# Kernel optimization log

Measured on AMD Instinct MI355X. Metric: run time of the kernel, lower is better.

Reference implementation:

```python
import jax, jax.numpy as jnp
import numpy as np
import math

B, T, D = 2, 512, 1024
H, HD = 16, 64
F = 4096
L = 2
R = 32
LOOP_DIM = 64
TEMB = 256
MAXIT = 8
TOPK = 0.55
EPS = 1e-6


def _ste(x, q):
    # straight-through estimator: forward = q, backward = identity
    return x + jax.lax.stop_gradient(q - x)


def bitlinear(x, w, topk_ratio=None):
    # BitNet b1.58 fake-quant: ternary weights (per-tensor absmean scale),
    # int8 per-token absmax activations; optional topk activation sparsity.
    s = jnp.mean(jnp.abs(w)) + 1e-8
    wq = _ste(w, jnp.clip(jnp.round(w / s), -1.0, 1.0) * s)
    if topk_ratio is not None:
        k = max(1, int(math.ceil(topk_ratio * x.shape[-1])))
        ax = jnp.abs(x)
        thr = jax.lax.top_k(ax, k)[0][..., -1:]
        x = jnp.where(ax >= thr, x, 0.0)
    a = jnp.maximum(jnp.max(jnp.abs(x), axis=-1, keepdims=True), 1e-8)
    xq = _ste(x, jnp.clip(jnp.round(x * (127.0 / a)), -128.0, 127.0) * (a / 127.0))
    return xq @ wq.T


def rmsnorm(x, w):
    return x * jax.lax.rsqrt(jnp.mean(x * x, axis=-1, keepdims=True) + EPS) * w


def _rope(x):
    # x: (B,H,T,HD)
    half = HD // 2
    inv = 1.0 / (10000.0 ** (jnp.arange(half, dtype=jnp.float32) / half))
    ang = jnp.arange(x.shape[2], dtype=jnp.float32)[:, None] * inv[None, :]
    cos, sin = jnp.cos(ang), jnp.sin(ang)
    x1, x2 = x[..., :half], x[..., half:]
    return jnp.concatenate([x1 * cos - x2 * sin, x1 * sin + x2 * cos], axis=-1)


def bitblock(h, n1, wq, wk, wv, wo, n2, wg, wu, wd):
    # pre-norm attention + SwiGLU FFN, all projections BitLinear
    b, t, _ = h.shape
    a_in = rmsnorm(h, n1)
    heads = lambda p: p.reshape(b, t, H, HD).transpose(0, 2, 1, 3)
    q = _rope(heads(bitlinear(a_in, wq)))
    k = _rope(heads(bitlinear(a_in, wk)))
    v = heads(bitlinear(a_in, wv))
    scores = jnp.einsum('bhqd,bhkd->bhqk', q, k) / math.sqrt(HD)
    mask = jnp.tril(jnp.ones((t, t), dtype=bool))
    attn = jax.nn.softmax(jnp.where(mask, scores, -1e9), axis=-1)
    o = jnp.einsum('bhqk,bhkd->bhqd', attn, v).transpose(0, 2, 1, 3).reshape(b, t, D)
    h = h + bitlinear(o, wo)
    f_in = rmsnorm(h, n2)
    h = h + bitlinear(jax.nn.silu(bitlinear(f_in, wg)) * bitlinear(f_in, wu), wd)
    return h


def loop_delta(i, t_emb, lp_w, lp2_w, lp2_b):
    # loop_index_inject: sinusoidal loop signal gated by t_emb, padded to D
    half = LOOP_DIM // 2
    frac = i / max(MAXIT - 1, 1)
    freqs = jnp.exp(-math.log(10000.0) * jnp.arange(half, dtype=jnp.float32) / half)
    ang = frac * freqs
    sig = jnp.concatenate([jnp.sin(ang), jnp.cos(ang)])  # (LOOP_DIM,)
    comb = sig[None, :] * (t_emb @ lp_w.T) + (t_emb @ lp2_w.T + lp2_b)  # (B,LOOP_DIM)
    return jnp.pad(comb, ((0, 0), (0, D - LOOP_DIM)))[:, None, :]  # (B,1,D)


def setup_inputs() -> dict:
    key = jax.random.key(0)
    ks = jax.random.split(key, 24)
    g = lambda k, shape, sc=0.02: sc * jax.random.normal(k, shape, dtype=jnp.float32)
    return {
        'x': jax.random.normal(ks[0], (B, T, D), dtype=jnp.float32),
        'e': jax.random.normal(ks[1], (B, T, D), dtype=jnp.float32),
        't_emb': jax.random.normal(ks[2], (B, TEMB), dtype=jnp.float32),
        'blk_norm1': jnp.ones((L, D), jnp.float32),
        'blk_wq': g(ks[3], (L, D, D)),
        'blk_wk': g(ks[4], (L, D, D)),
        'blk_wv': g(ks[5], (L, D, D)),
        'blk_wo': g(ks[6], (L, D, D)),
        'blk_norm2': jnp.ones((L, D), jnp.float32),
        'blk_wg': g(ks[7], (L, F, D)),
        'blk_wu': g(ks[8], (L, F, D)),
        'blk_wd': g(ks[9], (L, D, F)),
        'A_raw': 0.1 * jax.random.normal(ks[10], (D,), dtype=jnp.float32),
        'B_w': g(ks[11], (D, D)),
        'lora_down': g(ks[12], (R, D)),
        'lora_up': g(ks[13], (D, R)),
        'iter_gate': jnp.full((MAXIT,), 0.1, jnp.float32),
        'act_w': g(ks[14], (1, D)),
        'alpha': jnp.full((MAXIT,), 1.0 / L, jnp.float32),
        'loop_proj_w': g(ks[15], (LOOP_DIM, TEMB)),
        'loop_proj2_w': g(ks[16], (LOOP_DIM, TEMB)),
        'loop_proj2_b': jnp.zeros((LOOP_DIM,), jnp.float32),
        'loop_norm_w': jnp.ones((D,), jnp.float32),
        'n_loops': 8,
    }


def reference(x, e, t_emb, blk_norm1, blk_wq, blk_wk, blk_wv, blk_wo,
              blk_norm2, blk_wg, blk_wu, blk_wd, A_raw, B_w,
              lora_down, lora_up, iter_gate, act_w, alpha,
              loop_proj_w, loop_proj2_w, loop_proj2_b, loop_norm_w, n_loops):
    A_eff = 0.99 * jnp.tanh(A_raw)          # diagonal LTI, |A|<0.99
    Be = bitlinear(e, B_w)                  # loop-invariant anchor B(e)
    h = x
    h_out = x
    ws = []
    for i in range(int(n_loops)):
        h_in = rmsnorm(h + loop_delta(i, t_emb, loop_proj_w, loop_proj2_w, loop_proj2_b), loop_norm_w)
        bo = h_in
        for l in range(L):
            bo = bitblock(bo, blk_norm1[l], blk_wq[l], blk_wk[l], blk_wv[l], blk_wo[l],
                          blk_norm2[l], blk_wg[l], blk_wu[l], blk_wd[l])
        bo = alpha[i] * bo
        h = A_eff * h + Be + bo             # LTI injection
        h = h + iter_gate[i] * bitlinear(bitlinear(h, lora_down), lora_up, topk_ratio=TOPK)
        w = jax.nn.sigmoid(bitlinear(h, act_w))  # (B,T,1) soft ACT weight
        h_out = h_out + w * (h - h_out)     # incremental residual blend
        ws.append(w)
    ponder = jnp.mean(jnp.stack(ws))
    return h_out, ponder
```

## Files before the change

### kernel.cpp

```cpp
#include <hip/hip_runtime.h>
#include <stdint.h>

#define DEV static __device__ __forceinline__

typedef float f32x4 __attribute__((ext_vector_type(4)));
typedef int   i32x4 __attribute__((ext_vector_type(4)));
typedef unsigned short u16x8 __attribute__((ext_vector_type(8)));

DEV float bf2f(unsigned short u){ return __uint_as_float(((unsigned int)u)<<16); }
DEV unsigned short f2bfr(float f){
  unsigned int u = __float_as_uint(f);
  return (unsigned short)((u + 0x7FFF + ((u>>16)&1)) >> 16);
}
DEV signed char f2i8(float f){ return (signed char)(int)f; }

DEV float wredsum(float v){
#pragma unroll
  for (int o=32;o;o>>=1) v += __shfl_xor(v,o);
  return v;
}
DEV float wredmax(float v){
#pragma unroll
  for (int o=32;o;o>>=1) v = fmaxf(v,__shfl_xor(v,o));
  return v;
}
DEV float bredsum(float v, float* red){
  v = wredsum(v);
  if ((threadIdx.x&63)==0) red[threadIdx.x>>6] = v;
  __syncthreads();
  float r = red[0]+red[1]+red[2]+red[3];
  __syncthreads();
  return r;
}
DEV float bredmax(float v, float* red){
  v = wredmax(v);
  if ((threadIdx.x&63)==0) red[threadIdx.x>>6] = v;
  __syncthreads();
  float r = fmaxf(fmaxf(red[0],red[1]),fmaxf(red[2],red[3]));
  __syncthreads();
  return r;
}

__global__ void fill_k(float* p, int n, float v){
  int i = blockIdx.x*256 + threadIdx.x;
  if (i < n) p[i] = v;
}

__global__ __launch_bounds__(256) void setup_misc_k(const float* __restrict__ x,
                                                    float* __restrict__ h, float* __restrict__ ho,
                                                    const float* __restrict__ temb,
                                                    const float* __restrict__ lpw,
                                                    const float* __restrict__ lp2w,
                                                    const float* __restrict__ lp2b,
                                                    float* __restrict__ delta,
                                                    float* __restrict__ tab){
  __shared__ float red[4];
  int bid = blockIdx.x, t = threadIdx.x;
  if (bid < 1024){
    int i = bid*256 + t;
    float4 v = *(const float4*)(x + (size_t)i*4);
    *(float4*)(h  + (size_t)i*4) = v;
    *(float4*)(ho + (size_t)i*4) = v;
    if (i==0) ho[1048576] = 0.f;
  } else if (bid < 1152){
    int blk = bid - 1024;
    int b = blk >> 6, j = blk & 63;
    float te = temb[b*256 + t];
    float p1 = bredsum(te * lpw[j*256 + t], red);
    float p2 = bredsum(te * lp2w[j*256 + t], red);
    if (t < 8){
      int i = t;
      float frac = (float)i / 7.f;
      int jj = j & 31;
      float fr = expf(-logf(10000.f) * (float)jj * (1.f/32.f));
      float ang = frac * fr;
      float sig = (j < 32) ? sinf(ang) : cosf(ang);
      delta[i*128 + b*64 + j] = sig*p1 + p2 + lp2b[j];
    }
  } else {
    int i = (bid-1152)*256 + t;
    int tpos = i >> 5, d = i & 31;
    float inv = powf(10000.f, -(float)d * (1.f/32.f));
    float sv, cv; sincosf((float)tpos * inv, &sv, &cv);
    tab[i*2]   = cv;
    tab[i*2+1] = sv;
  }
}

struct WSetup {
  const float* src[18];
  signed char* dst[18];
  int mode[18];
};
DEV long n4of(int mat){ return mat<9 ? 262144 : (mat<15 ? 1048576 : (mat<17 ? 8192 : 256)); }

__global__ __launch_bounds__(256) void absmean_all_k(WSetup wsu, float* __restrict__ part){
  __shared__ float red[4];
  int bid = blockIdx.x, mat, seg;
  if (bid < 2304){ mat = bid >> 8; seg = bid & 255; }
  else if (bid < 8448){ mat = 9 + ((bid-2304) >> 10); seg = (bid-2304) & 1023; }
  else { mat = 15 + ((bid-8448) >> 8); seg = (bid-8448) & 255; }
  long n4 = n4of(mat);
  int segs = (mat >= 9 && mat < 15) ? 1024 : 256;
  long cnt = n4 / segs;
  const float4* p = (const float4*)wsu.src[mat] + (long)seg*cnt;
  float s0=0.f, s1=0.f, s2=0.f, s3=0.f;
  if (cnt >= 1024){
    long quar = cnt >> 2;
    const float4* p1 = p + quar;
    const float4* p2 = p + 2*quar;
    const float4* p3 = p + 3*quar;
    for (long j = threadIdx.x; j < quar; j += 256){
      float4 a = p[j], b = p1[j], c = p2[j], d = p3[j];
      s0 += fabsf(a.x)+fabsf(a.y)+fabsf(a.z)+fabsf(a.w);
      s1 += fabsf(b.x)+fabsf(b.y)+fabsf(b.z)+fabsf(b.w);
      s2 += fabsf(c.x)+fabsf(c.y)+fabsf(c.z)+fabsf(c.w);
      s3 += fabsf(d.x)+fabsf(d.y)+fabsf(d.z)+fabsf(d.w);
    }
  } else {
    for (long j = threadIdx.x; j < cnt; j += 256){
      float4 a = p[j];
      s0 += fabsf(a.x)+fabsf(a.y)+fabsf(a.z)+fabsf(a.w);
    }
  }
  float s = bredsum(s0+s1+s2+s3, red);
  if (threadIdx.x==0) part[(long)mat*1024 + seg] = s;
}

__global__ __launch_bounds__(256) void finalize_scales_k(const float* __restrict__ part,
                                                         float* __restrict__ scales){
  __shared__ float red[4];
  const long numel[18] = {1048576, 1048576,1048576, 1048576,1048576, 1048576,1048576,
                          1048576,1048576, 4194304,4194304, 4194304,4194304, 4194304,4194304,
                          32768, 32768, 1024};
  int t = threadIdx.x;
  for (int m=0;m<18;m++){
    int segs = (m >= 9 && m < 15) ? 1024 : 256;
    float v = 0.f;
    for (int j=t; j<segs; j+=256) v += part[(long)m*1024 + j];
    v = bredsum(v, red);
    if (t==0) scales[m] = v/(float)numel[m] + 1e-8f;
  }
  if (t==0){
    for (int l=0;l<2;l++){
      scales[18+l*3+0] = scales[1+l];
      scales[18+l*3+1] = scales[3+l];
      scales[18+l*3+2] = scales[5+l];
      scales[24+l*2+0] = scales[9+l];
      scales[24+l*2+1] = scales[11+l];
    }
  }
}

__global__ __launch_bounds__(256) void quantw_all_k(WSetup wsu, const float* __restrict__ scales){
  int bid = blockIdx.x;
  int mat = 0, c = 0;
  for (;;){
    int nb = mat<9 ? 256 : (mat<15 ? 1024 : (mat<17 ? 8 : 1));
    if (bid < c + nb) break;
    c += nb; mat++;
  }
  long seg = bid - c;
  long n4 = n4of(mat);
  float s = scales[mat];
  int md = wsu.mode[mat];
  const float4* src = (const float4*)wsu.src[mat];
  char4* dst = (char4*)wsu.dst[mat];
  long base = seg*1024;
#pragma unroll
  for (int k=0;k<4;k++){
    long i = base + k*256 + threadIdx.x;
    if (i < n4){
      float4 v = src[i];
      char4 q;
      q.x = f2i8(fminf(fmaxf(rintf(v.x/s), -1.f), 1.f));
      q.y = f2i8(fminf(fmaxf(rintf(v.y/s), -1.f), 1.f));
      q.z = f2i8(fminf(fmaxf(rintf(v.z/s), -1.f), 1.f));
      q.w = f2i8(fminf(fmaxf(rintf(v.w/s), -1.f), 1.f));
      if (md == 0) dst[i] = q;
      else {
        long r = i >> 8, cc = i & 255;
        dst[(((r<<1) | (md-1))<<8) | cc] = q;
      }
    }
  }
}

template<bool BF>
__global__ __launch_bounds__(256) void rowquant1k_k(const void* __restrict__ xin,
                                                    signed char* __restrict__ xq,
                                                    float* __restrict__ rs){
  __shared__ float red[4];
  int m = blockIdx.x, t = threadIdx.x;
  float v[4];
  if (BF){
    ushort4 u = *(const ushort4*)((const unsigned short*)xin + (size_t)m*1024 + t*4);
    v[0]=bf2f(u.x); v[1]=bf2f(u.y); v[2]=bf2f(u.z); v[3]=bf2f(u.w);
  } else {
    float4 f = *(const float4*)((const float*)xin + (size_t)m*1024 + t*4);
    v[0]=f.x; v[1]=f.y; v[2]=f.z; v[3]=f.w;
  }
  float am = fmaxf(fmaxf(fabsf(v[0]),fabsf(v[1])),fmaxf(fabsf(v[2]),fabsf(v[3])));
  am = bredmax(am, red);
  float a = fmaxf(am, 1e-8f), inv = 127.f/a;
  char4 q;
  q.x = f2i8(fminf(fmaxf(rintf(v[0]*inv),-128.f),127.f));
  q.y = f2i8(fminf(fmaxf(rintf(v[1]*inv),-128.f),127.f));
  q.z = f2i8(fminf(fmaxf(rintf(v[2]*inv),-128.f),127.f));
  q.w = f2i8(fminf(fmaxf(rintf(v[3]*inv),-128.f),127.f));
  *(char4*)(xq + (size_t)m*1024 + t*4) = q;
  if (t==0) rs[m] = a/127.f;
}

__global__ __launch_bounds__(256) void rowquant4k_k(const unsigned short* __restrict__ x,
                                                    signed char* __restrict__ xq,
                                                    float* __restrict__ rs){
  __shared__ float red[4];
  int m = blockIdx.x, t = threadIdx.x;
  const unsigned short* p = x + (size_t)m*4096 + t*16;
  u16x8 u0 = *(const u16x8*)p;
  u16x8 u1 = *(const u16x8*)(p + 8);
  float v[16];
#pragma unroll
  for (int j=0;j<8;j++){ v[j] = bf2f(u0[j]); v[j+8] = bf2f(u1[j]); }
  float am = 0.f;
#pragma unroll
  for (int j=0;j<16;j++) am = fmaxf(am, fabsf(v[j]));
  am = bredmax(am, red);
  float a = fmaxf(am, 1e-8f), inv = 127.f/a;
#pragma unroll
  for (int j=0;j<16;j+=4){
    char4 q;
    q.x = f2i8(fminf(fmaxf(rintf(v[j+0]*inv),-128.f),127.f));
    q.y = f2i8(fminf(fmaxf(rintf(v[j+1]*inv),-128.f),127.f));
    q.z = f2i8(fminf(fmaxf(rintf(v[j+2]*inv),-128.f),127.f));
    q.w = f2i8(fminf(fmaxf(rintf(v[j+3]*inv),-128.f),127.f));
    *(char4*)(xq + (size_t)m*4096 + t*16 + j) = q;
  }
  if (t==0) rs[m] = a/127.f;
}

__global__ __launch_bounds__(256) void loopnorm_quant_k(const float* __restrict__ h,
                                                        const float* __restrict__ delta,
                                                        const float* __restrict__ lnw,
                                                        const float* __restrict__ n1,
                                                        float* __restrict__ hin,
                                                        signed char* __restrict__ xq,
                                                        float* __restrict__ rs){
  __shared__ float red[4];
  int m = blockIdx.x, t = threadIdx.x;
  int b = m >> 9;
  float v[4];
  float4 f = *(const float4*)(h + (size_t)m*1024 + t*4);
  v[0]=f.x; v[1]=f.y; v[2]=f.z; v[3]=f.w;
  if (t < 16){
#pragma unroll
    for (int j=0;j<4;j++) v[j] += delta[b*64 + t*4 + j];
  }
  float ss = v[0]*v[0]+v[1]*v[1]+v[2]*v[2]+v[3]*v[3];
  ss = bredsum(ss, red);
  float r1 = rsqrtf(ss*(1.f/1024.f) + 1e-6f);
  float w4[4];
#pragma unroll
  for (int j=0;j<4;j++) w4[j] = v[j]*r1*lnw[t*4+j];
  float4 of; of.x=w4[0]; of.y=w4[1]; of.z=w4[2]; of.w=w4[3];
  *(float4*)(hin + (size_t)m*1024 + t*4) = of;
  float s2 = w4[0]*w4[0]+w4[1]*w4[1]+w4[2]*w4[2]+w4[3]*w4[3];
  s2 = bredsum(s2, red);
  float r2 = rsqrtf(s2*(1.f/1024.f) + 1e-6f);
  float y[4];
#pragma unroll
  for (int j=0;j<4;j++) y[j] = w4[j]*r2*n1[t*4+j];
  float am = fmaxf(fmaxf(fabsf(y[0]),fabsf(y[1])),fmaxf(fabsf(y[2]),fabsf(y[3])));
  am = bredmax(am, red);
  float a = fmaxf(am, 1e-8f), inv = 127.f/a;
  char4 q;
  q.x = f2i8(fminf(fmaxf(rintf(y[0]*inv),-128.f),127.f));
  q.y = f2i8(fminf(fmaxf(rintf(y[1]*inv),-128.f),127.f));
  q.z = f2i8(fminf(fmaxf(rintf(y[2]*inv),-128.f),127.f));
  q.w = f2i8(fminf(fmaxf(rintf(y[3]*inv),-128.f),127.f));
  *(char4*)(xq + (size_t)m*1024 + t*4) = q;
  if (t==0) rs[m] = a/127.f;
}

DEV f32x4 accfence(f32x4 c){ asm volatile("s_nop 7\n\ts_nop 7" : "+v"(c)); return c; }
DEV i32x4 accfencei(i32x4 c){ asm volatile("s_nop 7\n\ts_nop 7" : "+v"(c)); return c; }

template<bool SPLITK, bool GUSILU>
__global__ __launch_bounds__(256)
void gemm_i8(const signed char* __restrict__ A, const signed char* __restrict__ W,
             const float* __restrict__ rowsc, const float* __restrict__ wscv,
             const float* __restrict__ res, float* __restrict__ C, int N, int Kf, int Kc)
{
  __shared__ __align__(16) signed char As[3][8192];
  __shared__ __align__(16) signed char Bs[3][8192];
  const int tid = threadIdx.x;
  const int lane = tid & 63, wvid = tid >> 6;
  const int wr = wvid >> 1, wc = wvid & 1;
  const int bm = blockIdx.y, bn = blockIdx.x;

  const int r0 = (wvid<<4) + (lane>>2);
  const int sw = (((lane&3) ^ ((r0>>1)&3)) << 4);
  const long kstart = SPLITK ? (long)blockIdx.z * Kc : 0;
  const signed char* gA = A + (size_t)(bm*128 + r0)*Kf + kstart + sw;
  const signed char* gB = W + (size_t)(bn*128 + r0)*Kf + kstart + sw;
  const size_t row64 = (size_t)64*Kf;

#define STAGE(buf, koff) do { \
    __builtin_amdgcn_global_load_lds(gA + (koff),         &As[buf][(wvid<<10)],      16, 0, 0); \
    __builtin_amdgcn_global_load_lds(gA + (koff) + row64, &As[buf][(wvid<<10)+4096], 16, 0, 0); \
    __builtin_amdgcn_global_load_lds(gB + (koff),         &Bs[buf][(wvid<<10)],      16, 0, 0); \
    __builtin_amdgcn_global_load_lds(gB + (koff) + row64, &Bs[buf][(wvid<<10)+4096], 16, 0, 0); \
  } while(0)

  i32x4 acc[4][4] = {};
  const int rA = (wr<<6) + (lane&15);
  const int rB = (wc<<6) + (lane&15);
  const int psA = (((lane>>4) ^ (((lane&15)>>1)&3)) << 4);

  const int NT = Kc >> 6;
  STAGE(0, 0);
  STAGE(1, 64);
  int cur = 0, nxt = 1, nx2 = 2;
  for (int kt = 0; kt < NT; ++kt){
    const int k2 = kt + 2;
    const int kn = (k2 < NT) ? (k2<<6) : 0;
    STAGE(nx2, kn);
    asm volatile("s_waitcnt vmcnt(8)" ::: "memory");
    __builtin_amdgcn_s_barrier();
    asm volatile("" ::: "memory");
    i32x4 a[4], b[4];
    const signed char* Ab = As[cur];
    const signed char* Bb = Bs[cur];
#pragma unroll
    for (int mi=0;mi<4;mi++) a[mi] = *(const i32x4*)(Ab + (rA + mi*16)*64 + psA);
#pragma unroll
    for (int ni=0;ni<4;ni++) b[ni] = *(const i32x4*)(Bb + (rB + ni*16)*64 + psA);
#pragma unroll
    for (int mi=0;mi<4;mi++)
#pragma unroll
      for (int ni=0;ni<4;ni++)
        asm("v_mfma_i32_16x16x64_i8 %0, %1, %2, %0" : "+v"(acc[mi][ni]) : "v"(a[mi]), "v"(b[ni]));
    asm volatile("s_waitcnt lgkmcnt(0)" ::: "memory");
    __builtin_amdgcn_s_barrier();
    int tmp = cur; cur = nxt; nxt = nx2; nx2 = tmp;
  }
#undef STAGE

#pragma unroll
  for (int mi=0;mi<4;mi++)
#pragma unroll
    for (int ni=0;ni<4;ni++)
      acc[mi][ni] = accfencei(acc[mi][ni]);

  const int rif = (lane>>4)<<2;
  const int cif = lane&15;
  const int gcol0 = bn*128 + (wc<<6);

  if constexpr (SPLITK){
    float* P = C + (size_t)blockIdx.z * ((size_t)N << 10);
#pragma unroll
    for (int mi=0;mi<4;mi++)
#pragma unroll
      for (int r=0;r<4;r++){
        const int grow = bm*128 + (wr<<6) + mi*16 + rif + r;
#pragma unroll
        for (int ni=0;ni<4;ni++)
          P[(size_t)grow*N + gcol0 + ni*16 + cif] = (float)acc[mi][ni][r];
      }
    return;
  }

  if constexpr (GUSILU){
    const float sg = wscv[0], su = wscv[1];
    unsigned short* Cb = (unsigned short*)C;
#pragma unroll
    for (int mi=0;mi<4;mi++){
#pragma unroll
      for (int r=0;r<4;r++){
        const int grow = bm*128 + (wr<<6) + mi*16 + rif + r;
        const float rsc = rowsc[grow];
#pragma unroll
        for (int ni=0;ni<4;ni++){
          const int gcol = gcol0 + ni*16 + cif;
          float val = (float)acc[mi][ni][r] * rsc * ((gcol & 1) ? su : sg);
          float other = __shfl_xor(val, 1);
          if (!(lane & 1)){
            float g = val, u = other;
            float outv = g/(1.f+expf(-g))*u;
            Cb[(size_t)grow*4096 + (gcol>>1)] = f2bfr(outv);
          }
        }
      }
    }
    return;
  }

#pragma unroll
  for (int mi=0;mi<4;mi++){
#pragma unroll
    for (int r=0;r<4;r++){
      const int grow = bm*128 + (wr<<6) + mi*16 + rif + r;
      const float rsc = rowsc[grow];
#pragma unroll
      for (int ni=0;ni<4;ni++){
        const int gcol = gcol0 + ni*16 + cif;
        float vvv = (float)acc[mi][ni][r] * rsc * wscv[0];
        const size_t off = (size_t)grow*N + gcol;
        if (res) vvv += res[off];
        C[off] = vvv;
      }
    }
  }
}

__global__ __launch_bounds__(256)
void gemm_qkv128(const signed char* __restrict__ A, const signed char* __restrict__ W,
                 const float* __restrict__ rowsc, const float* __restrict__ wscv,
                 const float* __restrict__ tab, unsigned short* __restrict__ C)
{
  __shared__ __align__(16) signed char As[3][8192];
  __shared__ __align__(16) signed char Bs[3][8192];
  const int tid = threadIdx.x;
  const int lane = tid & 63, wvid = tid >> 6;
  const int wr = wvid >> 1, wc = wvid & 1;
  const int bm = blockIdx.y, bn = blockIdx.x;
  const int Kf = 1024;

  const int r0 = (wvid<<4) + (lane>>2);
  const int sw = (((lane&3) ^ ((r0>>1)&3)) << 4);
  const signed char* gA = A + (size_t)(bm*128 + r0)*Kf + sw;
  const signed char* gB = W + (size_t)(bn*128 + r0)*Kf + sw;
  const size_t row64 = (size_t)64*Kf;

#define STAGE(buf, koff) do { \
    __builtin_amdgcn_global_load_lds(gA + (koff),         &As[buf][(wvid<<10)],      16, 0, 0); \
    __builtin_amdgcn_global_load_lds(gA + (koff) + row64, &As[buf][(wvid<<10)+4096], 16, 0, 0); \
    __builtin_amdgcn_global_load_lds(gB + (koff),         &Bs[buf][(wvid<<10)],      16, 0, 0); \
    __builtin_amdgcn_global_load_lds(gB + (koff) + row64, &Bs[buf][(wvid<<10)+4096], 16, 0, 0); \
  } while(0)

  i32x4 acc[4][4] = {};
  const int rA = (wr<<6) + (lane&15);
  const int rB = (wc<<6) + (lane&15);
  const int psA = (((lane>>4) ^ (((lane&15)>>1)&3)) << 4);

  const int NT = 16;
  STAGE(0, 0);
  STAGE(1, 64);
  int cur = 0, nxt = 1, nx2 = 2;
  for (int kt = 0; kt < NT; ++kt){
    const int k2 = kt + 2;
    const int kn = (k2 < NT) ? (k2<<6) : 0;
    STAGE(nx2, kn);
    asm volatile("s_waitcnt vmcnt(8)" ::: "memory");
    __builtin_amdgcn_s_barrier();
    asm volatile("" ::: "memory");
    i32x4 a[4], b[4];
    const signed char* Ab = As[cur];
    const signed char* Bb = Bs[cur];
#pragma unroll
    for (int mi=0;mi<4;mi++) a[mi] = *(const i32x4*)(Ab + (rA + mi*16)*64 + psA);
#pragma unroll
    for (int ni=0;ni<4;ni++) b[ni] = *(const i32x4*)(Bb + (rB + ni*16)*64 + psA);
#pragma unroll
    for (int mi=0;mi<4;mi++)
#pragma unroll
      for (int ni=0;ni<4;ni++)
        asm("v_mfma_i32_16x16x64_i8 %0, %1, %2, %0" : "+v"(acc[mi][ni]) : "v"(a[mi]), "v"(b[ni]));
    asm volatile("s_waitcnt lgkmcnt(0)" ::: "memory");
    __builtin_amdgcn_s_barrier();
    int tmp = cur; cur = nxt; nxt = nx2; nx2 = tmp;
  }
#undef STAGE

#pragma unroll
  for (int mi=0;mi<4;mi++)
#pragma unroll
    for (int ni=0;ni<4;ni++)
      acc[mi][ni] = accfencei(acc[mi][ni]);

  const int rif = (lane>>4)<<2;
  const int cif = lane&15;
  const int gcol0 = bn*128 + (wc<<6);
  const int sec = gcol0 >> 10;
  const float wsc = wscv[sec] * ((sec==0) ? 0.125f : 1.f);

  if (sec < 2){
#pragma unroll
    for (int mi=0;mi<4;mi++){
#pragma unroll
      for (int r=0;r<4;r++){
        const int grow = bm*128 + (wr<<6) + mi*16 + rif + r;
        const float s = rowsc[grow] * wsc;
        const int tpos = grow & 511;
#pragma unroll
        for (int np=0;np<2;np++){
          const int d = np*16 + cif;
          float2 cs = *(const float2*)(tab + (size_t)((tpos<<5) + d)*2);
          float x1 = (float)acc[mi][np][r]   * s;
          float x2 = (float)acc[mi][np+2][r] * s;
          C[(size_t)grow*3072 + gcol0 + d]      = f2bfr(x1*cs.x - x2*cs.y);
          C[(size_t)grow*3072 + gcol0 + 32 + d] = f2bfr(x1*cs.y + x2*cs.x);
        }
      }
    }
  } else {
#pragma unroll
    for (int mi=0;mi<4;mi++){
#pragma unroll
      for (int r=0;r<4;r++){
        const int grow = bm*128 + (wr<<6) + mi*16 + rif + r;
        const float s = rowsc[grow] * wsc;
#pragma unroll
        for (int ni=0;ni<4;ni++)
          C[(size_t)grow*3072 + gcol0 + ni*16 + cif] = f2bfr((float)acc[mi][ni][r] * s);
      }
    }
  }
}

__global__ __launch_bounds__(256) void reduce4_k(const float* __restrict__ P,
                                                 const float* __restrict__ rowsc,
                                                 const float* __restrict__ wsc,
                                                 const float* __restrict__ res,
                                                 float* __restrict__ C){
  int m = blockIdx.x, t = threadIdx.x;
  float s0 = rowsc[m] * wsc[0];
  size_t off = (size_t)m*1024 + t*4;
  float4 a = *(const float4*)(P + off);
  float4 b = *(const float4*)(P + 1048576 + off);
  float4 c = *(const float4*)(P + 2097152 + off);
  float4 d = *(const float4*)(P + 3145728 + off);
  float4 o;
  o.x = (a.x+b.x+c.x+d.x)*s0;
  o.y = (a.y+b.y+c.y+d.y)*s0;
  o.z = (a.z+b.z+c.z+d.z)*s0;
  o.w = (a.w+b.w+c.w+d.w)*s0;
  if (res){
    float4 r = *(const float4*)(res + off);
    o.x += r.x; o.y += r.y; o.z += r.z; o.w += r.w;
  }
  *(float4*)(C + off) = o;
}

__global__ __launch_bounds__(256) void redq_norm_k(const float* __restrict__ P,
                                                   const float* rowsc,
                                                   const float* __restrict__ wsc,
                                                   const float* __restrict__ res,
                                                   const float* __restrict__ gamma,
                                                   float* __restrict__ Cout,
                                                   signed char* __restrict__ xq,
                                                   float* rs){
  __shared__ float red[4];
  int m = blockIdx.x, t = threadIdx.x;
  float s0 = rowsc[m] * wsc[0];
  size_t off = (size_t)m*1024 + t*4;
  float4 a = *(const float4*)(P + off);
  float4 b = *(const float4*)(P + 1048576 + off);
  float4 c = *(const float4*)(P + 2097152 + off);
  float4 d = *(const float4*)(P + 3145728 + off);
  float4 r4 = *(const float4*)(res + off);
  float v[4];
  v[0] = r4.x + (a.x+b.x+c.x+d.x)*s0;
  v[1] = r4.y + (a.y+b.y+c.y+d.y)*s0;
  v[2] = r4.z + (a.z+b.z+c.z+d.z)*s0;
  v[3] = r4.w + (a.w+b.w+c.w+d.w)*s0;
  float4 of; of.x=v[0]; of.y=v[1]; of.z=v[2]; of.w=v[3];
  *(float4*)(Cout + off) = of;
  float ss = v[0]*v[0]+v[1]*v[1]+v[2]*v[2]+v[3]*v[3];
  ss = bredsum(ss, red);
  float r1 = rsqrtf(ss*(1.f/1024.f) + 1e-6f);
  float y[4];
#pragma unroll
  for (int j=0;j<4;j++) y[j] = v[j]*r1*gamma[t*4+j];
  float am = fmaxf(fmaxf(fabsf(y[0]),fabsf(y[1])),fmaxf(fabsf(y[2]),fabsf(y[3])));
  am = bredmax(am, red);
  float aq = fmaxf(am, 1e-8f), inv = 127.f/aq;
  char4 q;
  q.x = f2i8(fminf(fmaxf(rintf(y[0]*inv),-128.f),127.f));
  q.y = f2i8(fminf(fmaxf(rintf(y[1]*inv),-128.f),127.f));
  q.z = f2i8(fminf(fmaxf(rintf(y[2]*inv),-128.f),127.f));
  q.w = f2i8(fminf(fmaxf(rintf(y[3]*inv),-128.f),127.f));
  *(char4*)(xq + (size_t)m*1024 + t*4) = q;
  if (t==0) rs[m] = aq/127.f;
}

__global__ __launch_bounds__(256) void redfin_k(const float* __restrict__ P,
                                                const float* __restrict__ rowsc,
                                                const float* __restrict__ wsc,
                                                const float* __restrict__ res,
                                                float* __restrict__ h,
                                                const float* __restrict__ Be,
                                                const float* __restrict__ Araw,
                                                const float* __restrict__ alpha, int it,
                                                const signed char* __restrict__ ldq,
                                                const float* __restrict__ sld,
                                                const signed char* __restrict__ luq,
                                                const float* __restrict__ slu,
                                                const signed char* __restrict__ actq,
                                                const float* __restrict__ sact,
                                                const float* __restrict__ ig,
                                                float* __restrict__ hout,
                                                float* __restrict__ ponder,
                                                const float* __restrict__ dnext,
                                                const float* __restrict__ lnw,
                                                const float* __restrict__ n1,
                                                float* __restrict__ hin,
                                                signed char* __restrict__ xqn,
                                                float* __restrict__ rsn,
                                                int doNext){
  __shared__ float red[4];
  __shared__ float xrow[1024];
  __shared__ float part[256];
  __shared__ float xs[32];
  __shared__ float sh_thr, sh_gs;
  int m = blockIdx.x, t = threadIdx.x;
  float al = alpha[it];
  float s0 = rowsc[m] * wsc[0];
  size_t off = (size_t)m*1024 + t*4;
  float4 a = *(const float4*)(P + off);
  float4 b = *(const float4*)(P + 1048576 + off);
  float4 c = *(const float4*)(P + 2097152 + off);
  float4 d = *(const float4*)(P + 3145728 + off);
  float4 r4 = *(const float4*)(res + off);
  float4 hh = *(const float4*)(h + off);
  float4 be = *(const float4*)(Be + off);
  float4 ar = *(const float4*)(Araw + t*4);
  float v[4];
  v[0] = 0.99f*tanhf(ar.x)*hh.x + be.x + al*(r4.x + (a.x+b.x+c.x+d.x)*s0);
  v[1] = 0.99f*tanhf(ar.y)*hh.y + be.y + al*(r4.y + (a.y+b.y+c.y+d.y)*s0);
  v[2] = 0.99f*tanhf(ar.z)*hh.z + be.z + al*(r4.z + (a.z+b.z+c.z+d.z)*s0);
  v[3] = 0.99f*tanhf(ar.w)*hh.w + be.w + al*(r4.w + (a.w+b.w+c.w+d.w)*s0);
  float am = fmaxf(fmaxf(fabsf(v[0]),fabsf(v[1])),fmaxf(fabsf(v[2]),fabsf(v[3])));
  am = bredmax(am, red);
  float aq = fmaxf(am, 1e-8f), inv = 127.f/aq;
#pragma unroll
  for (int j=0;j<4;j++) xrow[t*4+j] = fminf(fmaxf(rintf(v[j]*inv),-128.f),127.f);
  float rsv = aq/127.f;
  __syncthreads();
  {
    int r = t & 31, seg = t >> 5;
    const signed char* wrow = ldq + (size_t)r*1024 + seg*128;
    const float* xr = xrow + seg*128;
    float acc = 0.f;
    for (int k=0;k<128;k+=4){
      char4 w4 = *(const char4*)(wrow + k);
      acc += xr[k]*(float)w4.x + xr[k+1]*(float)w4.y + xr[k+2]*(float)w4.z + xr[k+3]*(float)w4.w;
    }
    part[t] = acc;
  }
  __syncthreads();
  if (t < 32){
    float s = 0.f;
    for (int sg=0; sg<8; sg++) s += part[sg*32 + t];
    xs[t] = s * rsv * (*sld);
  }
  __syncthreads();
  float val = 0.f, av = 0.f, amax = 0.f;
  if (t < 32){
    val = xs[t]; av = fabsf(val);
    int rank = 0;
    for (int j=0;j<32;j++){
      float aj = fabsf(xs[j]);
      amax = fmaxf(amax, aj);
      if (aj > av || (aj == av && j < t)) rank++;
    }
    if (rank == 17) sh_thr = av;
  }
  __syncthreads();
  if (t < 32){
    float a2 = fmaxf(amax, 1e-8f);
    float q = 0.f;
    if (av >= sh_thr) q = fminf(fmaxf(rintf(val*(127.f/a2)), -128.f), 127.f);
    xs[t] = q;
    if (t == 0) sh_gs = ig[it] * (*slu) * (a2/127.f);
  }
  __syncthreads();
  float gs = sh_gs;
  float hn[4];
  int n0 = t*4;
#pragma unroll
  for (int ni=0;ni<4;ni++){
    const signed char* lr = luq + (size_t)(n0+ni)*32;
    float dd = 0.f;
    for (int k=0;k<32;k+=4){
      char4 w4 = *(const char4*)(lr + k);
      dd += xs[k]*(float)w4.x + xs[k+1]*(float)w4.y + xs[k+2]*(float)w4.z + xs[k+3]*(float)w4.w;
    }
    hn[ni] = v[ni] + gs*dd;
  }
  float am2 = fmaxf(fmaxf(fabsf(hn[0]),fabsf(hn[1])),fmaxf(fabsf(hn[2]),fabsf(hn[3])));
  am2 = bredmax(am2, red);
  float a2 = fmaxf(am2, 1e-8f), inv2 = 127.f/a2;
  float zp = 0.f;
#pragma unroll
  for (int ni=0;ni<4;ni++){
    float q = fminf(fmaxf(rintf(hn[ni]*inv2),-128.f),127.f);
    zp += q * (float)actq[n0+ni];
  }
  zp = bredsum(zp, red);
  float z = zp * (a2/127.f) * (*sact);
  float wv = 1.f/(1.f+expf(-z));
#pragma unroll
  for (int ni=0;ni<4;ni++){
    size_t o2 = (size_t)m*1024 + n0+ni;
    float ho = hout[o2];
    hout[o2] = ho + wv*(hn[ni]-ho);
    h[o2] = hn[ni];
  }
  if (t==0) atomicAdd(ponder, wv * (1.f/8192.f));

  if (doNext){
    int b2 = m >> 9;
    float v2[4] = {hn[0], hn[1], hn[2], hn[3]};
    if (t < 16){
#pragma unroll
      for (int j=0;j<4;j++) v2[j] += dnext[b2*64 + t*4 + j];
    }
    float ss2 = v2[0]*v2[0]+v2[1]*v2[1]+v2[2]*v2[2]+v2[3]*v2[3];
    ss2 = bredsum(ss2, red);
    float r1 = rsqrtf(ss2*(1.f/1024.f) + 1e-6f);
    float w4[4];
#pragma unroll
    for (int j=0;j<4;j++) w4[j] = v2[j]*r1*lnw[t*4+j];
    float4 of; of.x=w4[0]; of.y=w4[1]; of.z=w4[2]; of.w=w4[3];
    *(float4*)(hin + off) = of;
    float s2 = w4[0]*w4[0]+w4[1]*w4[1]+w4[2]*w4[2]+w4[3]*w4[3];
    s2 = bredsum(s2, red);
    float r2 = rsqrtf(s2*(1.f/1024.f) + 1e-6f);
    float y[4];
#pragma unroll
    for (int j=0;j<4;j++) y[j] = w4[j]*r2*n1[t*4+j];
    float am3 = fmaxf(fmaxf(fabsf(y[0]),fabsf(y[1])),fmaxf(fabsf(y[2]),fabsf(y[3])));
    am3 = bredmax(am3, red);
    float aq3 = fmaxf(am3, 1e-8f), inv3 = 127.f/aq3;
    char4 q;
    q.x = f2i8(fminf(fmaxf(rintf(y[0]*inv3),-128.f),127.f));
    q.y = f2i8(fminf(fmaxf(rintf(y[1]*inv3),-128.f),127.f));
    q.z = f2i8(fminf(fmaxf(rintf(y[2]*inv3),-128.f),127.f));
    q.w = f2i8(fminf(fmaxf(rintf(y[3]*inv3),-128.f),127.f));
    *(char4*)(xqn + off) = q;
    if (t==0) rsn[m] = aq3/127.f;
  }
}

DEV int swz64(int r, int c){ return r*64 + (c ^ ((r&7)<<3)); }

__global__ __launch_bounds__(256) void attn_bf16_k(const unsigned short* __restrict__ qkv,
                                                   unsigned short* __restrict__ o){
  __shared__ __align__(16) unsigned short Qs[4096];
  __shared__ __align__(16) unsigned short Ks[4096];
  __shared__ __align__(16) unsigned short Vt[4096];
  __shared__ __align__(16) unsigned short Ps[4][1024];
  const int tid = threadIdx.x;
  const int lane = tid & 63, wv = tid >> 6;
  const int qt = blockIdx.x & 7, bh = blockIdx.x >> 3;
  const int b = bh >> 4, h = bh & 15;
  const int tokb = b*512;
  const int l15 = lane & 15, lh = lane >> 4;

  {
    int r = tid >> 2, c0 = (tid & 3) << 4;
    const unsigned short* s = qkv + (size_t)(tokb + qt*64 + r)*3072 + h*64 + c0;
    u16x8 f0 = *(const u16x8*)s, f1 = *(const u16x8*)(s+8);
    *(u16x8*)(Qs + swz64(r, c0))   = f0;
    *(u16x8*)(Qs + swz64(r, c0+8)) = f1;
  }

  float m_run[4] = {-1e30f,-1e30f,-1e30f,-1e30f};
  float l_run[4] = {0.f,0.f,0.f,0.f};
  f32x4 accO[4] = {};

  for (int kt = 0; kt <= qt; ++kt){
    __syncthreads();
    {
      int r = tid >> 2, c0 = (tid & 3) << 4;
      const unsigned short* s = qkv + (size_t)(tokb + kt*64 + r)*3072 + 1024 + h*64 + c0;
      u16x8 f0 = *(const u16x8*)s, f1 = *(const u16x8*)(s+8);
      *(u16x8*)(Ks + swz64(r, c0))   = f0;
      *(u16x8*)(Ks + swz64(r, c0+8)) = f1;
    }
    {
      int r0 = (tid >> 3) << 1, cv = (tid & 7) << 3;
      const unsigned short* s0 = qkv + (size_t)(tokb + kt*64 + r0)*3072 + 2048 + h*64 + cv;
      u16x8 a = *(const u16x8*)s0;
      u16x8 b2 = *(const u16x8*)(s0 + 3072);
#pragma unroll
      for (int j=0;j<8;j++){
        int d = cv + j;
        unsigned int pk = (unsigned int)a[j] | ((unsigned int)b2[j]<<16);
        *(unsigned int*)(Vt + swz64(d, r0)) = pk;
      }
    }
    __syncthreads();

    f32x4 s4[4] = {};
#pragma unroll
    for (int kc=0; kc<2; ++kc){
      i32x4 aq = *(const i32x4*)(Qs + swz64(wv*16 + l15, kc*32 + lh*8));
#pragma unroll
      for (int nt=0; nt<4; ++nt){
        i32x4 bk = *(const i32x4*)(Ks + swz64(nt*16 + l15, kc*32 + lh*8));
        asm("v_mfma_f32_16x16x32_bf16 %0, %1, %2, %0" : "+v"(s4[nt]) : "v"(aq), "v"(bk));
      }
    }
#pragma unroll
    for (int nt=0; nt<4; ++nt) s4[nt] = accfence(s4[nt]);

    const bool diag = (kt == qt);
    float sf[4];
#pragma unroll
    for (int r=0;r<4;r++){
      int rl = lh*4 + r;
      float mx = -1e30f;
#pragma unroll
      for (int nt=0; nt<4; ++nt){
        float v = s4[nt][r];
        if (diag && (nt*16 + l15) > (wv*16 + rl)) v = -1e30f;
        s4[nt][r] = v;
        mx = fmaxf(mx, v);
      }
      mx = fmaxf(mx, __shfl_xor(mx,1));
      mx = fmaxf(mx, __shfl_xor(mx,2));
      mx = fmaxf(mx, __shfl_xor(mx,4));
      mx = fmaxf(mx, __shfl_xor(mx,8));
      float mn = fmaxf(m_run[r], mx);
      sf[r] = __expf(m_run[r] - mn);
      m_run[r] = mn;
      float ps = 0.f;
#pragma unroll
      for (int nt=0; nt<4; ++nt){
        float p = __expf(s4[nt][r] - mn);
        ps += p;
        Ps[wv][swz64(rl, nt*16 + l15)] = f2bfr(p);
      }
      ps += __shfl_xor(ps,1); ps += __shfl_xor(ps,2);
      ps += __shfl_xor(ps,4); ps += __shfl_xor(ps,8);
      l_run[r] = l_run[r]*sf[r] + ps;
    }
#pragma unroll
    for (int dt=0; dt<4; ++dt){
#pragma unroll
      for (int r=0;r<4;r++) accO[dt][r] *= sf[r];
      accO[dt] = accfence(accO[dt]);
    }
#pragma unroll
    for (int kc=0; kc<2; ++kc){
      i32x4 pa = *(const i32x4*)(Ps[wv] + swz64(l15, kc*32 + lh*8));
#pragma unroll
      for (int dt=0; dt<4; ++dt){
        i32x4 vb3 = *(const i32x4*)(Vt + swz64(dt*16 + l15, kc*32 + lh*8));
        asm("v_mfma_f32_16x16x32_bf16 %0, %1, %2, %0" : "+v"(accO[dt]) : "v"(pa), "v"(vb3));
      }
    }
  }
#pragma unroll
  for (int dt=0; dt<4; ++dt) accO[dt] = accfence(accO[dt]);
#pragma unroll
  for (int r=0;r<4;r++){
    float invl = 1.f / l_run[r];
    int row = qt*64 + wv*16 + lh*4 + r;
    unsigned short* op = o + (size_t)(tokb + row)*1024 + h*64 + l15;
#pragma unroll
    for (int dt=0; dt<4; ++dt)
      op[dt*16] = f2bfr(accO[dt][r] * invl);
  }
}

extern "C" void kernel_launch(void* const* d_in, const int* in_sizes, int n_in,
                              void* d_out, int out_size, void* d_ws, size_t ws_size,
                              hipStream_t stream)
{
  (void)in_sizes; (void)n_in;
  const float* x     = (const float*)d_in[0];
  const float* e     = (const float*)d_in[1];
  const float* temb  = (const float*)d_in[2];
  const float* bn1   = (const float*)d_in[3];
  const float* bwq   = (const float*)d_in[4];
  const float* bwk   = (const float*)d_in[5];
  const float* bwv   = (const float*)d_in[6];
  const float* bwo   = (const float*)d_in[7];
  const float* bn2   = (const float*)d_in[8];
  const float* bwg   = (const float*)d_in[9];
  const float* bwu   = (const float*)d_in[10];
  const float* bwd   = (const float*)d_in[11];
  const float* Araw  = (const float*)d_in[12];
  const float* Bw    = (const float*)d_in[13];
  const float* ldw   = (const float*)d_in[14];
  const float* luw   = (const float*)d_in[15];
  const float* ig    = (const float*)d_in[16];
  const float* actw  = (const float*)d_in[17];
  const float* alph  = (const float*)d_in[18];
  const float* lpw   = (const float*)d_in[19];
  const float* lp2w  = (const float*)d_in[20];
  const float* lp2b  = (const float*)d_in[21];
  const float* lnw   = (const float*)d_in[22];

  char* ws = (char*)d_ws;
  float* out = (float*)d_out;
  const size_t WS_NEEDED = 94600704ull;
  if (ws_size < WS_NEEDED){
    fill_k<<<(out_size+255)/256,256,0,stream>>>(out, out_size, 1.0e9f);
    return;
  }

  signed char* qw_qkv = (signed char*)(ws + 0);
  signed char* qw_wo  = (signed char*)(ws + 6291456);
  signed char* qw_gu  = (signed char*)(ws + 8388608);
  signed char* qw_wd  = (signed char*)(ws + 25165824);
  signed char* qw_bw  = (signed char*)(ws + 33554432);
  signed char* qw_ld  = (signed char*)(ws + 34603008);
  signed char* qw_lu  = (signed char*)(ws + 34635776);
  signed char* qw_act = (signed char*)(ws + 34668544);
  float* scales = (float*)(ws + 34669568);
  float* delta  = (float*)(ws + 34688512);
  float* hbuf   = (float*)(ws + 34692608);
  float* Bebuf  = (float*)(ws + 38886912);
  float* bufX   = (float*)(ws + 43081216);
  float* bufY   = (float*)(ws + 47275520);
  float* gub    = (float*)(ws + 51469824);
  unsigned short* qkv_bf = (unsigned short*)(ws + 76635648);
  unsigned short* obuf = (unsigned short*)(ws + 85024256);
  signed char* xq1k = (signed char*)(ws + 89218560);
  float* rs1k   = (float*)(ws + 90267136);
  signed char* xqm  = (signed char*)(ws + 90271232);
  float* rsm    = (float*)(ws + 94465536);
  float* ropetab= (float*)(ws + 94469632);
  float* part   = gub;

  WSetup wsu;
  wsu.src[0]=Bw;
  wsu.src[1]=bwq; wsu.src[2]=bwq+1048576;
  wsu.src[3]=bwk; wsu.src[4]=bwk+1048576;
  wsu.src[5]=bwv; wsu.src[6]=bwv+1048576;
  wsu.src[7]=bwo; wsu.src[8]=bwo+1048576;
  wsu.src[9]=bwg; wsu.src[10]=bwg+4194304;
  wsu.src[11]=bwu; wsu.src[12]=bwu+4194304;
  wsu.src[13]=bwd; wsu.src[14]=bwd+4194304;
  wsu.src[15]=ldw; wsu.src[16]=luw; wsu.src[17]=actw;
  wsu.dst[0]=qw_bw;
  wsu.dst[1]=qw_qkv;             wsu.dst[2]=qw_qkv+3145728;
  wsu.dst[3]=qw_qkv+1048576;     wsu.dst[4]=qw_qkv+3145728+1048576;
  wsu.dst[5]=qw_qkv+2097152;     wsu.dst[6]=qw_qkv+3145728+2097152;
  wsu.dst[7]=qw_wo;              wsu.dst[8]=qw_wo+1048576;
  wsu.dst[9]=qw_gu;              wsu.dst[10]=qw_gu+8388608;
  wsu.dst[11]=qw_gu;             wsu.dst[12]=qw_gu+8388608;
  wsu.dst[13]=qw_wd;             wsu.dst[14]=qw_wd+4194304;
  wsu.dst[15]=qw_ld; wsu.dst[16]=qw_lu; wsu.dst[17]=qw_act;
  for (int i=0;i<18;i++) wsu.mode[i]=0;
  wsu.mode[9]=1;  wsu.mode[10]=1;
  wsu.mode[11]=2; wsu.mode[12]=2;

  absmean_all_k<<<9216,256,0,stream>>>(wsu, part);
  finalize_scales_k<<<1,256,0,stream>>>(part, scales);
  quantw_all_k<<<8465,256,0,stream>>>(wsu, scales);

  setup_misc_k<<<1216,256,0,stream>>>(x, hbuf, out, temb, lpw, lp2w, lp2b, delta, ropetab);

  rowquant1k_k<false><<<1024,256,0,stream>>>(e, xq1k, rs1k);
  { dim3 g(8,8,4); gemm_i8<true,false><<<g,256,0,stream>>>(xq1k, qw_bw, nullptr, nullptr, nullptr, gub, 1024, 1024, 256); }
  reduce4_k<<<1024,256,0,stream>>>(gub, rs1k, scales+0, nullptr, Bebuf);

  for (int it=0; it<8; ++it){
    if (it==0)
      loopnorm_quant_k<<<1024,256,0,stream>>>(hbuf, delta, lnw, bn1, bufX, xq1k, rs1k);
    for (int l=0;l<2;l++){
      { dim3 g(24,8); gemm_qkv128<<<g,256,0,stream>>>(xq1k, qw_qkv + (size_t)l*3145728, rs1k, scales+18+l*3, ropetab, qkv_bf); }
      attn_bf16_k<<<256,256,0,stream>>>(qkv_bf, obuf);
      rowquant1k_k<true><<<1024,256,0,stream>>>(obuf, xq1k, rs1k);
      { dim3 g(8,8,4); gemm_i8<true,false><<<g,256,0,stream>>>(xq1k, qw_wo + (size_t)l*1048576, nullptr, nullptr, nullptr, gub, 1024, 1024, 256); }
      redq_norm_k<<<1024,256,0,stream>>>(gub, rs1k, scales+7+l, bufX, bn2 + (size_t)l*1024, bufY, xq1k, rs1k);
      { dim3 g(64,8); gemm_i8<false,true><<<g,256,0,stream>>>(xq1k, qw_gu + (size_t)l*8388608, rs1k, scales+24+l*2, nullptr, gub, 8192, 1024, 1024); }
      rowquant4k_k<<<1024,256,0,stream>>>((const unsigned short*)gub, xqm, rsm);
      { dim3 g(8,8,4); gemm_i8<true,false><<<g,256,0,stream>>>(xqm, qw_wd + (size_t)l*4194304, nullptr, nullptr, nullptr, gub, 1024, 4096, 1024); }
      if (l==0){
        redq_norm_k<<<1024,256,0,stream>>>(gub, rsm, scales+13, bufY, bn1 + 1024, bufX, xq1k, rs1k);
      } else {
        redfin_k<<<1024,256,0,stream>>>(gub, rsm, scales+14, bufY, hbuf, Bebuf, Araw, alph, it,
                                        qw_ld, scales+15, qw_lu, scales+16, qw_act, scales+17,
                                        ig, out, out + 1048576,
                                        delta + (it+1 < 8 ? (it+1)*128 : 0), lnw, bn1, bufX, xq1k, rs1k,
                                        (it < 7) ? 1 : 0);
      }
    }
  }
}
```

Before: 1.965 ms.

## Split causal attention over two KV halves and fuse merge with row quantization

The attention kernel now launches twice as many blocks, each covering half of the causal key-tile range for a query tile. Each block writes unnormalized fp32 partial outputs plus per-row running max and sum. A new merge kernel combines the two partials with log-sum-exp weights and applies int8 row quantization in the same pass, replacing the separate rowquant kernel. The aim is to even out the causal load imbalance, where the last query tiles do far more work than the first, and to raise parallelism on the GPU. In exchange, the partials are written and read as fp32, which moves more memory than the old bf16 output.

```diff
diff --git a/kernel.cpp b/kernel.cpp
--- a/kernel.cpp
+++ b/kernel.cpp
@@ -747,15 +747,18 @@
 
 DEV int swz64(int r, int c){ return r*64 + (c ^ ((r&7)<<3)); }
 
-__global__ __launch_bounds__(256) void attn_bf16_k(const unsigned short* __restrict__ qkv,
-                                                   unsigned short* __restrict__ o){
+__global__ __launch_bounds__(256) void attn_split_k(const unsigned short* __restrict__ qkv,
+                                                    float* __restrict__ Opart,
+                                                    float* __restrict__ ml){
   __shared__ __align__(16) unsigned short Qs[4096];
   __shared__ __align__(16) unsigned short Ks[4096];
   __shared__ __align__(16) unsigned short Vt[4096];
   __shared__ __align__(16) unsigned short Ps[4][1024];
   const int tid = threadIdx.x;
   const int lane = tid & 63, wv = tid >> 6;
-  const int qt = blockIdx.x & 7, bh = blockIdx.x >> 3;
+  const int bidl = blockIdx.x & 255;
+  const int z = blockIdx.x >> 8;
+  const int qt = bidl & 7, bh = bidl >> 3;
   const int b = bh >> 4, h = bh & 15;
   const int tokb = b*512;
   const int l15 = lane & 15, lh = lane >> 4;
@@ -772,7 +775,12 @@
   float l_run[4] = {0.f,0.f,0.f,0.f};
   f32x4 accO[4] = {};
 
-  for (int kt = 0; kt <= qt; ++kt){
+  const int nt = qt + 1;
+  const int half = (nt + 1) >> 1;
+  const int kA = z ? half : 0;
+  const int kB = z ? nt : half;
+
+  for (int kt = kA; kt < kB; ++kt){
     __syncthreads();
     {
       int r = tid >> 2, c0 = (tid & 3) << 4;
@@ -800,13 +808,13 @@
     for (int kc=0; kc<2; ++kc){
       i32x4 aq = *(const i32x4*)(Qs + swz64(wv*16 + l15, kc*32 + lh*8));
 #pragma unroll
-      for (int nt=0; nt<4; ++nt){
-        i32x4 bk = *(const i32x4*)(Ks + swz64(nt*16 + l15, kc*32 + lh*8));
-        asm("v_mfma_f32_16x16x32_bf16 %0, %1, %2, %0" : "+v"(s4[nt]) : "v"(aq), "v"(bk));
-      }
-    }
-#pragma unroll
-    for (int nt=0; nt<4; ++nt) s4[nt] = accfence(s4[nt]);
+      for (int nt2=0; nt2<4; ++nt2){
+        i32x4 bk = *(const i32x4*)(Ks + swz64(nt2*16 + l15, kc*32 + lh*8));
+        asm("v_mfma_f32_16x16x32_bf16 %0, %1, %2, %0" : "+v"(s4[nt2]) : "v"(aq), "v"(bk));
+      }
+    }
+#pragma unroll
+    for (int nt2=0; nt2<4; ++nt2) s4[nt2] = accfence(s4[nt2]);
 
     const bool diag = (kt == qt);
     float sf[4];
@@ -815,10 +823,10 @@
       int rl = lh*4 + r;
       float mx = -1e30f;
 #pragma unroll
-      for (int nt=0; nt<4; ++nt){
-        float v = s4[nt][r];
-        if (diag && (nt*16 + l15) > (wv*16 + rl)) v = -1e30f;
-        s4[nt][r] = v;
+      for (int nt2=0; nt2<4; ++nt2){
+        float v = s4[nt2][r];
+        if (diag && (nt2*16 + l15) > (wv*16 + rl)) v = -1e30f;
+        s4[nt2][r] = v;
         mx = fmaxf(mx, v);
       }
       mx = fmaxf(mx, __shfl_xor(mx,1));
@@ -830,10 +838,10 @@
       m_run[r] = mn;
       float ps = 0.f;
 #pragma unroll
-      for (int nt=0; nt<4; ++nt){
-        float p = __expf(s4[nt][r] - mn);
+      for (int nt2=0; nt2<4; ++nt2){
+        float p = __expf(s4[nt2][r] - mn);
         ps += p;
-        Ps[wv][swz64(rl, nt*16 + l15)] = f2bfr(p);
+        Ps[wv][swz64(rl, nt2*16 + l15)] = f2bfr(p);
       }
       ps += __shfl_xor(ps,1); ps += __shfl_xor(ps,2);
       ps += __shfl_xor(ps,4); ps += __shfl_xor(ps,8);
@@ -857,15 +865,51 @@
   }
 #pragma unroll
   for (int dt=0; dt<4; ++dt) accO[dt] = accfence(accO[dt]);
+  float* Op = Opart + ((size_t)z << 20);
 #pragma unroll
   for (int r=0;r<4;r++){
-    float invl = 1.f / l_run[r];
-    int row = qt*64 + wv*16 + lh*4 + r;
-    unsigned short* op = o + (size_t)(tokb + row)*1024 + h*64 + l15;
+    int row = tokb + qt*64 + wv*16 + lh*4 + r;
+    float* op = Op + (size_t)row*1024 + h*64 + l15;
 #pragma unroll
     for (int dt=0; dt<4; ++dt)
-      op[dt*16] = f2bfr(accO[dt][r] * invl);
-  }
+      op[dt*16] = accO[dt][r];
+    if (l15 == 0){
+      float2 v2 = make_float2(m_run[r], l_run[r]);
+      *(float2*)(ml + ((size_t)(z*16 + h)*1024 + row)*2) = v2;
+    }
+  }
+}
+
+__global__ __launch_bounds__(256) void attn_merge_quant_k(const float* __restrict__ Opart,
+                                                          const float* __restrict__ ml,
+                                                          signed char* __restrict__ xq,
+                                                          float* __restrict__ rs){
+  __shared__ float red[4];
+  int m = blockIdx.x, t = threadIdx.x;
+  int head = t >> 4;
+  float2 ml0 = *(const float2*)(ml + ((size_t)head*1024 + m)*2);
+  float2 ml1 = *(const float2*)(ml + ((size_t)(16 + head)*1024 + m)*2);
+  float mm = fmaxf(ml0.x, ml1.x);
+  float w0 = __expf(ml0.x - mm), w1 = __expf(ml1.x - mm);
+  float invl = 1.f / (ml0.y*w0 + ml1.y*w1);
+  size_t off = (size_t)m*1024 + t*4;
+  float4 o0 = *(const float4*)(Opart + off);
+  float4 o1 = *(const float4*)(Opart + 1048576 + off);
+  float v[4];
+  v[0] = (o0.x*w0 + o1.x*w1)*invl;
+  v[1] = (o0.y*w0 + o1.y*w1)*invl;
+  v[2] = (o0.z*w0 + o1.z*w1)*invl;
+  v[3] = (o0.w*w0 + o1.w*w1)*invl;
+  float am = fmaxf(fmaxf(fabsf(v[0]),fabsf(v[1])),fmaxf(fabsf(v[2]),fabsf(v[3])));
+  am = bredmax(am, red);
+  float a = fmaxf(am, 1e-8f), inv = 127.f/a;
+  char4 q;
+  q.x = f2i8(fminf(fmaxf(rintf(v[0]*inv),-128.f),127.f));
+  q.y = f2i8(fminf(fmaxf(rintf(v[1]*inv),-128.f),127.f));
+  q.z = f2i8(fminf(fmaxf(rintf(v[2]*inv),-128.f),127.f));
+  q.w = f2i8(fminf(fmaxf(rintf(v[3]*inv),-128.f),127.f));
+  *(char4*)(xq + (size_t)m*1024 + t*4) = q;
+  if (t==0) rs[m] = a/127.f;
 }
 
 extern "C" void kernel_launch(void* const* d_in, const int* in_sizes, int n_in,
@@ -921,7 +965,7 @@
   float* bufY   = (float*)(ws + 47275520);
   float* gub    = (float*)(ws + 51469824);
   unsigned short* qkv_bf = (unsigned short*)(ws + 76635648);
-  unsigned short* obuf = (unsigned short*)(ws + 85024256);
+  float* mlbuf  = (float*)(ws + 85024256);
   signed char* xq1k = (signed char*)(ws + 89218560);
   float* rs1k   = (float*)(ws + 90267136);
   signed char* xqm  = (signed char*)(ws + 90271232);
@@ -967,8 +1011,8 @@
       loopnorm_quant_k<<<1024,256,0,stream>>>(hbuf, delta, lnw, bn1, bufX, xq1k, rs1k);
     for (int l=0;l<2;l++){
       { dim3 g(24,8); gemm_qkv128<<<g,256,0,stream>>>(xq1k, qw_qkv + (size_t)l*3145728, rs1k, scales+18+l*3, ropetab, qkv_bf); }
-      attn_bf16_k<<<256,256,0,stream>>>(qkv_bf, obuf);
-      rowquant1k_k<true><<<1024,256,0,stream>>>(obuf, xq1k, rs1k);
+      attn_split_k<<<512,256,0,stream>>>(qkv_bf, gub, mlbuf);
+      attn_merge_quant_k<<<1024,256,0,stream>>>(gub, mlbuf, xq1k, rs1k);
       { dim3 g(8,8,4); gemm_i8<true,false><<<g,256,0,stream>>>(xq1k, qw_wo + (size_t)l*1048576, nullptr, nullptr, nullptr, gub, 1024, 1024, 256); }
       redq_norm_k<<<1024,256,0,stream>>>(gub, rs1k, scales+7+l, bufX, bn2 + (size_t)l*1024, bufY, xq1k, rs1k);
       { dim3 g(64,8); gemm_i8<false,true><<<g,256,0,stream>>>(xq1k, qw_gu + (size_t)l*8388608, rs1k, scales+24+l*2, nullptr, gub, 8192, 1024, 1024); }
```

After: 1.854 ms. -5.6%, faster.
